# Kernel optimization log

Hardware: AMD Instinct MI355X
Metric: run time of the kernel (lower is better)

## Reference

```python
import jax, jax.numpy as jnp
import numpy as np

DIM = 512; H = 8; TEMP_LEN = 16; TARGET_LEN = 22
NT = TEMP_LEN ** 2          # 256 temp tokens
NS = TARGET_LEN ** 2        # 484 target tokens
N = NT + NS                 # 740
HD = DIM // H
SCALE = HD ** -0.5
EPS = 1e-5
B = 16


def _bias_index(L):
    coords = np.stack(np.meshgrid(np.arange(L), np.arange(L), indexing='ij')).reshape(2, -1)
    rel = (coords[:, :, None] - coords[:, None, :]).transpose(1, 2, 0)  # [L^2, L^2, 2]
    rel[..., 0] += L - 1
    rel[..., 1] += L - 1
    rel[..., 0] *= 2 * L - 1
    return jnp.asarray(rel.sum(-1))  # [L^2, L^2] indices into (2L-1)^2 table

TEMP_IDX = _bias_index(TEMP_LEN)
TARGET_IDX = _bias_index(TARGET_LEN)


def setup_inputs() -> dict:
    key = jax.random.key(0)
    ctr = iter(range(100))
    def nrm(shape, s=1.0):
        return jax.random.normal(jax.random.fold_in(key, next(ctr)), shape, jnp.float32) * s
    def uni(shape):
        return jax.random.uniform(jax.random.fold_in(key, next(ctr)), shape, jnp.float32, 0.5, 1.5)
    d = {'x': nrm((B, N, DIM))}
    for nm in ('q', 'k', 'v'):
        d[f'conv_{nm}_w'] = nrm((DIM, 1, 3, 3), 0.2)   # depthwise 3x3, groups=DIM
        d[f'bn_{nm}_g'] = 1.0 + nrm((DIM,), 0.1)
        d[f'bn_{nm}_b'] = nrm((DIM,), 0.1)
        d[f'bn_{nm}_m'] = nrm((DIM,), 0.1)
        d[f'bn_{nm}_v'] = uni((DIM,))
    for nm in ('q', 'k', 'v', 'p'):
        d[f'w{nm}'] = nrm((DIM, DIM), DIM ** -0.5)
        d[f'b{nm}'] = nrm((DIM,), 0.01)
    d['rpb_target'] = nrm(((2 * TARGET_LEN - 1) ** 2, H), 0.0002)
    d['rpb_temp'] = nrm(((2 * TEMP_LEN - 1) ** 2, 1), 0.0002)
    d['tt_bias'] = nrm((H, 1, NT), 0.0002)       # temp_target_bias_table
    d['tg_tm_bias'] = nrm((H, NS, 1), 0.0002)    # target_temp_bias_table
    return d


def _dwconv_bn(z, w, g, b, m, v):
    # z: [B, C, Hh, Ww]; depthwise conv + BatchNorm2d (inference stats)
    y = jax.lax.conv_general_dilated(z, w, (1, 1), ((1, 1), (1, 1)),
                                     dimension_numbers=('NCHW', 'OIHW', 'NCHW'),
                                     feature_group_count=DIM)
    inv = (g * jax.lax.rsqrt(v + EPS))[None, :, None, None]
    return (y - m[None, :, None, None]) * inv + b[None, :, None, None]


def reference(x, conv_q_w, bn_q_g, bn_q_b, bn_q_m, bn_q_v,
              conv_k_w, bn_k_g, bn_k_b, bn_k_m, bn_k_v,
              conv_v_w, bn_v_g, bn_v_b, bn_v_m, bn_v_v,
              wq, bq, wk, bk, wv, bv, wp, bp,
              rpb_target, rpb_temp, tt_bias, tg_tm_bias):
    Bb = x.shape[0]
    to_img = lambda t, L: t.transpose(0, 2, 1).reshape(Bb, DIM, L, L)
    to_seq = lambda t: t.reshape(Bb, DIM, -1).transpose(0, 2, 1)
    ti = to_img(x[:, :NT], TEMP_LEN)
    tg = to_img(x[:, NT:], TARGET_LEN)

    def conv_branch(w, g, b, m, v):
        return jnp.concatenate([to_seq(_dwconv_bn(ti, w, g, b, m, v)),
                                to_seq(_dwconv_bn(tg, w, g, b, m, v))], axis=1)

    q = conv_branch(conv_q_w, bn_q_g, bn_q_b, bn_q_m, bn_q_v) @ wq + bq
    k = conv_branch(conv_k_w, bn_k_g, bn_k_b, bn_k_m, bn_k_v) @ wk + bk
    v = conv_branch(conv_v_w, bn_v_g, bn_v_b, bn_v_m, bn_v_v) @ wv + bv

    heads = lambda t: t.reshape(Bb, -1, H, HD).transpose(0, 2, 1, 3)
    qtm, ktm, vtm = heads(q[:, :NT]), heads(k[:, :NT]), heads(v[:, :NT])
    qta, kh, vh = heads(q[:, NT:]), heads(k), heads(v)

    # gathered relative-position bias tables
    target_bias = rpb_target[TARGET_IDX.reshape(-1)].reshape(NS, NS, H).transpose(2, 0, 1)  # [H,NS,NS]
    temp_bias = rpb_temp[TEMP_IDX.reshape(-1)].reshape(NT, NT, 1).transpose(2, 0, 1)        # [1,NT,NT]
    padding = tt_bias + tg_tm_bias                                                          # [H,NS,NT]
    rel = jnp.concatenate([padding, target_bias], axis=2)                                   # [H,NS,N]

    # target -> all attention
    attn = jax.nn.softmax(jnp.einsum('bhqd,bhkd->bhqk', qta, kh) * SCALE + rel, axis=-1)
    out_t = jnp.einsum('bhqk,bhkd->bhqd', attn, vh).transpose(0, 2, 1, 3).reshape(Bb, NS, DIM)

    # temp -> temp attention (bias broadcast over heads)
    attn2 = jax.nn.softmax(jnp.einsum('bhqd,bhkd->bhqk', qtm, ktm) * SCALE + temp_bias, axis=-1)
    out_m = jnp.einsum('bhqk,bhkd->bhqd', attn2, vtm).transpose(0, 2, 1, 3).reshape(Bb, NT, DIM)

    return jnp.concatenate([out_m, out_t], axis=1) @ wp + bp
```

## Files before the change

kernel.cpp:

```cpp
#include <hip/hip_runtime.h>
#include <hip/hip_bf16.h>

typedef unsigned short u16;
typedef unsigned int u32;
typedef __attribute__((ext_vector_type(8))) short short8;
typedef __attribute__((ext_vector_type(4))) float f32x4;

#define NTOK 740
#define NTMP 256
#define NTGT 484
#define DM   512
#define MH   8
#define MROWS 11840
#define KPAD 768
#define LOG2E 1.4426950408889634f

__device__ __forceinline__ float b2f(u16 u) {
    union { unsigned int i; float f; } x; x.i = ((unsigned int)u) << 16; return x.f;
}
__device__ __forceinline__ u16 f2b(float f) {
    union { float f; unsigned int i; } x; x.f = f;
    unsigned int r = x.i + 0x7FFFu + ((x.i >> 16) & 1u);
    return (u16)(r >> 16);
}
__device__ __forceinline__ u32 pk2(float a, float b) {
    union { __hip_bfloat162 h; u32 u; } p;
    p.h = __float22bfloat162_rn(float2{a, b});
    return p.u;
}
__device__ __forceinline__ float fexp2(float x) {
    return __builtin_amdgcn_exp2f(x);
}
struct alignas(8) us4 { u16 x, y, z, w; };

__device__ __forceinline__ void gload16(const void* g, void* l) {
    __builtin_amdgcn_global_load_lds(
        (const __attribute__((address_space(1))) void*)g,
        (__attribute__((address_space(3))) void*)l, 16, 0, 0);
}

__global__ __launch_bounds__(256) void transpose4(const float* __restrict__ w0,
                                                  const float* __restrict__ w1,
                                                  const float* __restrict__ w2,
                                                  const float* __restrict__ w3,
                                                  u16* __restrict__ wTbase) {
    __shared__ float t[32][33];
    const int z = blockIdx.z;
    const float* W = z == 0 ? w0 : z == 1 ? w1 : z == 2 ? w2 : w3;
    u16* WT = wTbase + (size_t)z * 262144;
    int bx = blockIdx.x, by = blockIdx.y;
    int tx = threadIdx.x;
    for (int i = threadIdx.y; i < 32; i += 8)
        t[i][tx] = W[(size_t)(by * 32 + i) * 512 + bx * 32 + tx];
    __syncthreads();
    for (int i = threadIdx.y; i < 32; i += 8)
        WT[(size_t)(bx * 32 + i) * 512 + by * 32 + tx] = f2b(t[tx][i]);
}

__global__ __launch_bounds__(512) void prep_conv3(
    const float* __restrict__ cw0, const float* __restrict__ g0, const float* __restrict__ bb0,
    const float* __restrict__ m0, const float* __restrict__ v0,
    const float* __restrict__ cw1, const float* __restrict__ g1, const float* __restrict__ bb1,
    const float* __restrict__ m1, const float* __restrict__ v1,
    const float* __restrict__ cw2, const float* __restrict__ g2, const float* __restrict__ bb2,
    const float* __restrict__ m2, const float* __restrict__ v2,
    float* __restrict__ cwfb, float* __restrict__ shb) {
    const int tap = blockIdx.x, br = blockIdx.y, c = threadIdx.x;
    const float* cw = br == 0 ? cw0 : br == 1 ? cw1 : cw2;
    const float* g  = br == 0 ? g0  : br == 1 ? g1  : g2;
    const float* bb = br == 0 ? bb0 : br == 1 ? bb1 : bb2;
    const float* m  = br == 0 ? m0  : br == 1 ? m1  : m2;
    const float* v  = br == 0 ? v0  : br == 1 ? v1  : v2;
    const float inv = g[c] * rsqrtf(v[c] + 1e-5f);
    cwfb[(br * 9 + tap) * DM + c] = cw[c * 9 + tap] * inv;
    if (tap == 0) shb[br * DM + c] = bb[c] - m[c] * inv;
}

__global__ __launch_bounds__(256) void conv_bn3(
    const float* __restrict__ x,
    const float* __restrict__ cwfb, const float* __restrict__ shb,
    u16* __restrict__ o0, u16* __restrict__ o1, u16* __restrict__ o2) {
    const int bn = blockIdx.x * 2 + (threadIdx.x >> 7);
    const int c = (threadIdx.x & 127) * 4;
    const int b = bn / NTOK, n = bn % NTOK;
    const bool tmp = n < NTMP;
    const int L = tmp ? 16 : 22, base = tmp ? 0 : NTMP, p = n - base;
    const int ph = p / L, pw = p % L;
    float4 xv[9];
#pragma unroll
    for (int tap = 0; tap < 9; ++tap) {
        const int dh = tap / 3 - 1, dw = tap % 3 - 1;
        const int h2 = ph + dh, w2 = pw + dw;
        const bool ok = (h2 >= 0 && h2 < L && w2 >= 0 && w2 < L);
        xv[tap] = ok ? *(const float4*)(x + (size_t)(b * NTOK + base + h2 * L + w2) * DM + c)
                     : float4{0.f, 0.f, 0.f, 0.f};
    }
    const size_t o = (size_t)bn * DM + c;
    u16* out[3] = {o0, o1, o2};
#pragma unroll
    for (int br = 0; br < 3; ++br) {
        float4 acc = *(const float4*)(shb + br * DM + c);
#pragma unroll
        for (int tap = 0; tap < 9; ++tap) {
            const float4 wv = *(const float4*)(cwfb + (br * 9 + tap) * DM + c);
            acc.x = fmaf(wv.x, xv[tap].x, acc.x);
            acc.y = fmaf(wv.y, xv[tap].y, acc.y);
            acc.z = fmaf(wv.z, xv[tap].z, acc.z);
            acc.w = fmaf(wv.w, xv[tap].w, acc.w);
        }
        us4 r;
        r.x = f2b(acc.x); r.y = f2b(acc.y); r.z = f2b(acc.z); r.w = f2b(acc.w);
        *(us4*)(out[br] + o) = r;
    }
}

#define GEMM_BODY(A, BT)                                                             \
    const int tid = threadIdx.x;                                                     \
    const int gm0 = blockIdx.x * 64;                                                 \
    const int gn0 = blockIdx.y * 128;                                                \
    const int lane = tid & 63, w = tid >> 6;                                         \
    const int lr = lane & 15, lg = lane >> 4;                                        \
    const int wm = (w >> 1) * 32, wn = (w & 1) * 64;                                 \
    const int srow4 = lane >> 2;                                                     \
    const int sc = (lane & 3) ^ (srow4 & 3);                                         \
    const u16* asrc  = A  + (size_t)(gm0 + w * 16 + srow4) * 512 + sc * 8;           \
    const u16* bsrc0 = BT + (size_t)(gn0 + w * 32 + srow4) * 512 + sc * 8;           \
    const u16* bsrc1 = BT + (size_t)(gn0 + w * 32 + 16 + srow4) * 512 + sc * 8;      \
    f32x4 acc[2][4] = {};                                                            \
    gload16(asrc, &As[0][w * 512]);                                                  \
    gload16(bsrc0, &Bs[0][w * 1024]);                                                \
    gload16(bsrc1, &Bs[0][w * 1024 + 512]);                                          \
    for (int kt = 0; kt < 16; ++kt) {                                                \
        const int cur = kt & 1;                                                      \
        if (kt < 15) {                                                               \
            gload16(asrc + (kt + 1) * 32, &As[cur ^ 1][w * 512]);                    \
            gload16(bsrc0 + (kt + 1) * 32, &Bs[cur ^ 1][w * 1024]);                  \
            gload16(bsrc1 + (kt + 1) * 32, &Bs[cur ^ 1][w * 1024 + 512]);            \
            asm volatile("s_waitcnt vmcnt(3)" ::: "memory");                         \
        } else {                                                                     \
            asm volatile("s_waitcnt vmcnt(0)" ::: "memory");                         \
        }                                                                            \
        __syncthreads();                                                             \
        short8 af[2], bfr[4];                                                        \
        _Pragma("unroll")                                                            \
        for (int i = 0; i < 2; ++i)                                                  \
            af[i] = *(const short8*)&As[cur][(wm + i * 16 + lr) * 32 + (lg ^ (lr & 3)) * 8]; \
        _Pragma("unroll")                                                            \
        for (int j = 0; j < 4; ++j)                                                  \
            bfr[j] = *(const short8*)&Bs[cur][(wn + j * 16 + lr) * 32 + (lg ^ (lr & 3)) * 8]; \
        _Pragma("unroll")                                                            \
        for (int i = 0; i < 2; ++i)                                                  \
            _Pragma("unroll")                                                        \
            for (int j = 0; j < 4; ++j)                                              \
                acc[i][j] = __builtin_amdgcn_mfma_f32_16x16x32_bf16(af[i], bfr[j], acc[i][j], 0, 0, 0); \
        __syncthreads();                                                             \
    }

__global__ __launch_bounds__(256) void gemm_qkv(
    const u16* __restrict__ Aq, const u16* __restrict__ Ak, const u16* __restrict__ Av,
    const u16* __restrict__ wTb, const float* __restrict__ bq,
    const float* __restrict__ bk, const float* __restrict__ bv,
    u16* __restrict__ qout, u16* __restrict__ kout, u16* __restrict__ vbT, int zbase) {
    __shared__ u16 As[2][64 * 32];
    __shared__ u16 Bs[2][128 * 32];
    const int z = blockIdx.z + zbase;
    const u16* A = z == 0 ? Aq : z == 1 ? Ak : Av;
    const u16* BT = wTb + (size_t)z * 262144;
    const float* bias = z == 0 ? bq : z == 1 ? bk : bv;
    GEMM_BODY(A, BT)
    u16* lin = z == 0 ? qout : kout;
#pragma unroll
    for (int i = 0; i < 2; ++i)
#pragma unroll
        for (int j = 0; j < 4; ++j) {
            const int gc = gn0 + wn + j * 16 + lr;
            const float bvl = bias[gc];
#pragma unroll
            for (int r = 0; r < 4; ++r) {
                const int gr = gm0 + wm + i * 16 + lg * 4 + r;
                const float val = acc[i][j][r] + bvl;
                if (z == 2) {
                    const int b2 = gr / NTOK, k = gr - b2 * NTOK;
                    const int hh = gc >> 6, d = gc & 63;
                    vbT[((size_t)(b2 * MH + hh) * 64 + d) * KPAD + k] = f2b(val);
                } else {
                    lin[(size_t)gr * 512 + gc] = f2b(val);
                }
            }
        }
}

__global__ __launch_bounds__(256) void gemm_out(const u16* __restrict__ Ain,
                                                const u16* __restrict__ BTin,
                                                const float* __restrict__ bias,
                                                float* __restrict__ C) {
    __shared__ u16 As[2][64 * 32];
    __shared__ u16 Bs[2][128 * 32];
    GEMM_BODY(Ain, BTin)
#pragma unroll
    for (int i = 0; i < 2; ++i)
#pragma unroll
        for (int j = 0; j < 4; ++j) {
            const int gc = gn0 + wn + j * 16 + lr;
            const float bvl = bias[gc];
#pragma unroll
            for (int r = 0; r < 4; ++r) {
                const int gr = gm0 + wm + i * 16 + lg * 4 + r;
                C[(size_t)gr * 512 + gc] = acc[i][j][r] + bvl;
            }
        }
}

__global__ __launch_bounds__(256) void build_bias_t(const float* __restrict__ rpb_t,
                                                    const float* __restrict__ tt,
                                                    const float* __restrict__ tg,
                                                    u16* __restrict__ btab) {
    const int q = blockIdx.x, h = blockIdx.y;
    const int qh = q / 22, qw = q % 22;
    const float tgv = tg[h * NTGT + q];
    for (int k = threadIdx.x; k < KPAD; k += 256) {
        float val;
        if (k < NTMP) val = (tt[h * NTMP + k] + tgv) * LOG2E;
        else if (k < NTOK) {
            const int kj = k - NTMP, kh = kj / 22, kw = kj % 22;
            val = rpb_t[((qh - kh + 21) * 43 + (qw - kw + 21)) * MH + h] * LOG2E;
        } else val = -1e30f;
        btab[((size_t)(h * NTGT + q)) * KPAD + k] = f2b(val);
    }
}
__global__ __launch_bounds__(256) void build_bias_m(const float* __restrict__ rpb_m,
                                                    u16* __restrict__ mtab) {
    const int q = blockIdx.x, k = threadIdx.x;
    const int qh = q >> 4, qw = q & 15, kh = k >> 4, kw = k & 15;
    mtab[q * 256 + k] = f2b(rpb_m[(qh - kh + 15) * 31 + (qw - kw + 15)] * LOG2E);
}

__global__ __launch_bounds__(256) void attn_all(const u16* __restrict__ qb,
                                                const u16* __restrict__ kb,
                                                const u16* __restrict__ vbT,
                                                const u16* __restrict__ btab,
                                                const u16* __restrict__ mtab,
                                                u16* __restrict__ attb) {
    __shared__ u16 Ks[2][32][64];
    __shared__ u16 VTs[2][64][32];
    __shared__ u16 Pb[2][4][16][32];

    int wg = blockIdx.x + 6 * (blockIdx.y + 8 * blockIdx.z);
    wg = (wg & 7) * 96 + (wg >> 3);
    const int bx = wg % 6;
    const int hb = wg / 6;
    const int h = hb & 7, b = hb >> 3;

    const bool tgt = bx < 4;
    const int q0 = (tgt ? bx : bx - 4) * 128;
    const int NKr = tgt ? NTOK : NTMP;
    const int NCH = tgt ? 24 : 8;
    const int QTOT = tgt ? NTGT : NTMP;
    const int QOFF = tgt ? NTMP : 0;
    const int TK = tgt ? KPAD : 256;
    const int tid = threadIdx.x;
    const int w = tid >> 6, lane = tid & 63;
    const int lq = lane & 15, lg = lane >> 4;
    const int fq = (lq & 3) ^ ((lq >> 2) & 3);
    const size_t brow = (size_t)b * NTOK;
    const float SCL = 0.125f * LOG2E;

    int qA = q0 + w * 16 + lq;       if (qA > QTOT - 1) qA = QTOT - 1;
    int qB = q0 + 64 + w * 16 + lq;  if (qB > QTOT - 1) qB = QTOT - 1;
    const u16* tbase = tgt ? (btab + (size_t)h * NTGT * KPAD) : mtab;
    const u16* trowA = tbase + (size_t)qA * TK;
    const u16* trowB = tbase + (size_t)qB * TK;

    short8 qfA[2], qfB[2];
#pragma unroll
    for (int dc = 0; dc < 2; ++dc) {
        qfA[dc] = *(const short8*)(qb + (brow + QOFF + qA) * DM + h * 64 + dc * 32 + lg * 8);
        qfB[dc] = *(const short8*)(qb + (brow + QOFF + qB) * DM + h * 64 + dc * 32 + lg * 8);
    }

    const int krow = tid >> 3, ksc = tid & 7;
    const int vrow = tid >> 2, vsc = tid & 3;
    const int fv = (vrow & 3) ^ ((vrow >> 2) & 3);
    const size_t vbase = (size_t)(b * MH + h) * 64 * KPAD;
    const u16* kptr2 = kb + brow * DM + h * 64 + (ksc ^ (krow & 7)) * 8;
    const u16* vptr2 = vbT + vbase + (size_t)vrow * KPAD + (vsc ^ fv) * 8;
    const int NKm1 = NKr - 1;

    float mrunA = -1e30f, lrunA = 0.f, mrunB = -1e30f, lrunB = 0.f;
    f32x4 oTA[4] = {}, oTB[4] = {};

    {
        const int keyc = krow < NKm1 ? krow : NKm1;
        gload16(kptr2 + (size_t)keyc * DM, &Ks[0][w * 8][0]);
        gload16(vptr2, &VTs[0][w * 16][0]);
    }
    us4 bcA0 = *(const us4*)(trowA + lg * 4);
    us4 bcA1 = *(const us4*)(trowA + 16 + lg * 4);
    us4 bcB0 = *(const us4*)(trowB + lg * 4);
    us4 bcB1 = *(const us4*)(trowB + 16 + lg * 4);
    asm volatile("s_waitcnt vmcnt(0)" ::: "memory");
    __syncthreads();

    for (int kc = 0; kc < NCH; ++kc) {
        const int cur = kc & 1, nxt = cur ^ 1;
        const bool more = (kc + 1 < NCH);
        us4 bnA0 = {0,0,0,0}, bnA1 = {0,0,0,0}, bnB0 = {0,0,0,0}, bnB1 = {0,0,0,0};
        if (more) {
            const int key = (kc + 1) * 32 + krow;
            const int keyc = key < NKm1 ? key : NKm1;
            gload16(kptr2 + (size_t)keyc * DM, &Ks[nxt][w * 8][0]);
            gload16(vptr2 + (kc + 1) * 32, &VTs[nxt][w * 16][0]);
            bnA0 = *(const us4*)(trowA + (kc + 1) * 32 + lg * 4);
            bnA1 = *(const us4*)(trowA + (kc + 1) * 32 + 16 + lg * 4);
            bnB0 = *(const us4*)(trowB + (kc + 1) * 32 + lg * 4);
            bnB1 = *(const us4*)(trowB + (kc + 1) * 32 + 16 + lg * 4);
        }

        f32x4 sA0 = {}, sA1 = {}, sB0 = {}, sB1 = {};
        __builtin_amdgcn_s_setprio(1);
#pragma unroll
        for (int dc = 0; dc < 2; ++dc) {
            short8 a0 = *(const short8*)&Ks[cur][lq][((dc * 4 + lg) ^ (lq & 7)) * 8];
            short8 a1 = *(const short8*)&Ks[cur][16 + lq][((dc * 4 + lg) ^ (lq & 7)) * 8];
            sA0 = __builtin_amdgcn_mfma_f32_16x16x32_bf16(a0, qfA[dc], sA0, 0, 0, 0);
            sB0 = __builtin_amdgcn_mfma_f32_16x16x32_bf16(a0, qfB[dc], sB0, 0, 0, 0);
            sA1 = __builtin_amdgcn_mfma_f32_16x16x32_bf16(a1, qfA[dc], sA1, 0, 0, 0);
            sB1 = __builtin_amdgcn_mfma_f32_16x16x32_bf16(a1, qfB[dc], sB1, 0, 0, 0);
        }
        __builtin_amdgcn_s_setprio(0);

        {
            float sv[8];
            sv[0] = fmaf(sA0[0], SCL, b2f(bcA0.x)); sv[1] = fmaf(sA0[1], SCL, b2f(bcA0.y));
            sv[2] = fmaf(sA0[2], SCL, b2f(bcA0.z)); sv[3] = fmaf(sA0[3], SCL, b2f(bcA0.w));
            sv[4] = fmaf(sA1[0], SCL, b2f(bcA1.x)); sv[5] = fmaf(sA1[1], SCL, b2f(bcA1.y));
            sv[6] = fmaf(sA1[2], SCL, b2f(bcA1.z)); sv[7] = fmaf(sA1[3], SCL, b2f(bcA1.w));
            float cm = sv[0];
#pragma unroll
            for (int i = 1; i < 8; ++i) cm = fmaxf(cm, sv[i]);
            cm = fmaxf(cm, __shfl_xor(cm, 16));
            cm = fmaxf(cm, __shfl_xor(cm, 32));
            if (!__all(cm <= mrunA)) {
                const float mnew = fmaxf(mrunA, cm);
                const float alpha = fexp2(mrunA - mnew);
#pragma unroll
                for (int t = 0; t < 4; ++t)
#pragma unroll
                    for (int r = 0; r < 4; ++r) oTA[t][r] *= alpha;
                lrunA *= alpha;
                mrunA = mnew;
            }
            float pv[8], psum = 0.f;
#pragma unroll
            for (int i = 0; i < 8; ++i) { pv[i] = fexp2(sv[i] - mrunA); psum += pv[i]; }
            const int c0 = (((lg >> 1) ^ fq) & 3) * 8 + (lg & 1) * 4;
            const int c1 = (((2 + (lg >> 1)) ^ fq) & 3) * 8 + (lg & 1) * 4;
            *(uint2*)&Pb[0][w][lq][c0] = uint2{pk2(pv[0], pv[1]), pk2(pv[2], pv[3])};
            *(uint2*)&Pb[0][w][lq][c1] = uint2{pk2(pv[4], pv[5]), pk2(pv[6], pv[7])};
            psum += __shfl_xor(psum, 16);
            psum += __shfl_xor(psum, 32);
            lrunA += psum;
        }
        {
            float sv[8];
            sv[0] = fmaf(sB0[0], SCL, b2f(bcB0.x)); sv[1] = fmaf(sB0[1], SCL, b2f(bcB0.y));
            sv[2] = fmaf(sB0[2], SCL, b2f(bcB0.z)); sv[3] = fmaf(sB0[3], SCL, b2f(bcB0.w));
            sv[4] = fmaf(sB1[0], SCL, b2f(bcB1.x)); sv[5] = fmaf(sB1[1], SCL, b2f(bcB1.y));
            sv[6] = fmaf(sB1[2], SCL, b2f(bcB1.z)); sv[7] = fmaf(sB1[3], SCL, b2f(bcB1.w));
            float cm = sv[0];
#pragma unroll
            for (int i = 1; i < 8; ++i) cm = fmaxf(cm, sv[i]);
            cm = fmaxf(cm, __shfl_xor(cm, 16));
            cm = fmaxf(cm, __shfl_xor(cm, 32));
            if (!__all(cm <= mrunB)) {
                const float mnew = fmaxf(mrunB, cm);
                const float alpha = fexp2(mrunB - mnew);
#pragma unroll
                for (int t = 0; t < 4; ++t)
#pragma unroll
                    for (int r = 0; r < 4; ++r) oTB[t][r] *= alpha;
                lrunB *= alpha;
                mrunB = mnew;
            }
            float pv[8], psum = 0.f;
#pragma unroll
            for (int i = 0; i < 8; ++i) { pv[i] = fexp2(sv[i] - mrunB); psum += pv[i]; }
            const int c0 = (((lg >> 1) ^ fq) & 3) * 8 + (lg & 1) * 4;
            const int c1 = (((2 + (lg >> 1)) ^ fq) & 3) * 8 + (lg & 1) * 4;
            *(uint2*)&Pb[1][w][lq][c0] = uint2{pk2(pv[0], pv[1]), pk2(pv[2], pv[3])};
            *(uint2*)&Pb[1][w][lq][c1] = uint2{pk2(pv[4], pv[5]), pk2(pv[6], pv[7])};
            psum += __shfl_xor(psum, 16);
            psum += __shfl_xor(psum, 32);
            lrunB += psum;
        }

        asm volatile("s_waitcnt lgkmcnt(0)" ::: "memory");

        short8 pfA = *(const short8*)&Pb[0][w][lq][((lg ^ fq) & 3) * 8];
        short8 pfB = *(const short8*)&Pb[1][w][lq][((lg ^ fq) & 3) * 8];
        __builtin_amdgcn_s_setprio(1);
#pragma unroll
        for (int t = 0; t < 4; ++t) {
            short8 vf = *(const short8*)&VTs[cur][t * 16 + lq][((lg ^ fq) & 3) * 8];
            oTA[t] = __builtin_amdgcn_mfma_f32_16x16x32_bf16(vf, pfA, oTA[t], 0, 0, 0);
            oTB[t] = __builtin_amdgcn_mfma_f32_16x16x32_bf16(vf, pfB, oTB[t], 0, 0, 0);
        }
        __builtin_amdgcn_s_setprio(0);

        bcA0 = bnA0; bcA1 = bnA1; bcB0 = bnB0; bcB1 = bnB1;
        asm volatile("s_waitcnt vmcnt(0)" ::: "memory");
        __syncthreads();
    }

    {
        const float linv = 1.f / lrunA;
        const int qrow = q0 + w * 16 + lq;
        if (qrow < QTOT) {
            u16* op = attb + (brow + QOFF + qrow) * DM + h * 64;
#pragma unroll
            for (int t = 0; t < 4; ++t)
                *(uint2*)(op + t * 16 + lg * 4) =
                    uint2{pk2(oTA[t][0] * linv, oTA[t][1] * linv),
                          pk2(oTA[t][2] * linv, oTA[t][3] * linv)};
        }
    }
    {
        const float linv = 1.f / lrunB;
        const int qrow = q0 + 64 + w * 16 + lq;
        if (qrow < QTOT) {
            u16* op = attb + (brow + QOFF + qrow) * DM + h * 64;
#pragma unroll
            for (int t = 0; t < 4; ++t)
                *(uint2*)(op + t * 16 + lg * 4) =
                    uint2{pk2(oTB[t][0] * linv, oTB[t][1] * linv),
                          pk2(oTB[t][2] * linv, oTB[t][3] * linv)};
        }
    }
}

extern "C" void kernel_launch(void* const* d_in, const int* in_sizes, int n_in,
                              void* d_out, int out_size, void* d_ws, size_t ws_size,
                              hipStream_t stream) {
    const float* x = (const float*)d_in[0];
    const float* convw[3] = {(const float*)d_in[1], (const float*)d_in[6], (const float*)d_in[11]};
    const float* bng[3]   = {(const float*)d_in[2], (const float*)d_in[7], (const float*)d_in[12]};
    const float* bnb[3]   = {(const float*)d_in[3], (const float*)d_in[8], (const float*)d_in[13]};
    const float* bnm[3]   = {(const float*)d_in[4], (const float*)d_in[9], (const float*)d_in[14]};
    const float* bnv[3]   = {(const float*)d_in[5], (const float*)d_in[10], (const float*)d_in[15]};
    const float* w[4]     = {(const float*)d_in[16], (const float*)d_in[18], (const float*)d_in[20], (const float*)d_in[22]};
    const float* bias[4]  = {(const float*)d_in[17], (const float*)d_in[19], (const float*)d_in[21], (const float*)d_in[23]};
    const float* rpb_t = (const float*)d_in[24];
    const float* rpb_m = (const float*)d_in[25];
    const float* tt    = (const float*)d_in[26];
    const float* tg    = (const float*)d_in[27];

    char* ws = (char*)d_ws;
    u16* wTb = (u16*)ws;
    const size_t SEQ = (size_t)MROWS * DM * 2;
    u16* cbq  = (u16*)(ws + 2097152);
    u16* cbk  = (u16*)(ws + 2097152 + SEQ);
    u16* cbv  = (u16*)(ws + 2097152 + 2 * SEQ);
    u16* kbuf = (u16*)(ws + 2097152 + 3 * SEQ);
    u16* vbT  = (u16*)(ws + 2097152 + 4 * SEQ);
    u16* btab = (u16*)(ws + 2097152 + 4 * SEQ + 12582912);
    u16* mtab = (u16*)(ws + 2097152 + 4 * SEQ + 12582912 + 5947392);
    float* cwf = (float*)(ws + 2097152 + 4 * SEQ + 12582912 + 5947392 + 131072);
    float* shf = cwf + 3 * 9 * DM;
    const size_t off_q2 = 2097152 + 4 * SEQ + 12582912 + 5947392 + 131072 + 61440;
    const bool merged = ws_size >= off_q2 + SEQ;
    u16* qbuf = merged ? (u16*)(ws + off_q2) : cbv;
    u16* attb = cbq;

    transpose4<<<dim3(16, 16, 4), dim3(32, 8), 0, stream>>>(w[0], w[1], w[2], w[3], wTb);
    prep_conv3<<<dim3(9, 3), 512, 0, stream>>>(
        convw[0], bng[0], bnb[0], bnm[0], bnv[0],
        convw[1], bng[1], bnb[1], bnm[1], bnv[1],
        convw[2], bng[2], bnb[2], bnm[2], bnv[2], cwf, shf);
    build_bias_t<<<dim3(NTGT, MH), 256, 0, stream>>>(rpb_t, tt, tg, btab);
    build_bias_m<<<256, 256, 0, stream>>>(rpb_m, mtab);

    conv_bn3<<<MROWS / 2, 256, 0, stream>>>(x, cwf, shf, cbq, cbk, cbv);

    if (merged) {
        gemm_qkv<<<dim3(185, 4, 3), 256, 0, stream>>>(cbq, cbk, cbv, wTb,
                                                      bias[0], bias[1], bias[2],
                                                      qbuf, kbuf, vbT, 0);
    } else {
        gemm_qkv<<<dim3(185, 4, 1), 256, 0, stream>>>(cbq, cbk, cbv, wTb,
                                                      bias[0], bias[1], bias[2],
                                                      qbuf, kbuf, vbT, 2);
        gemm_qkv<<<dim3(185, 4, 2), 256, 0, stream>>>(cbq, cbk, cbv, wTb,
                                                      bias[0], bias[1], bias[2],
                                                      qbuf, kbuf, vbT, 0);
    }

    attn_all<<<dim3(6, 8, 16), 256, 0, stream>>>(qbuf, kbuf, vbT, btab, mtab, attb);

    gemm_out<<<dim3(185, 4), 256, 0, stream>>>(attb, wTb + 3 * 262144, bias[3], (float*)d_out);
}
```

Baseline: 179.1 us.

## Fuse prep kernels into one launch and remap GEMM blocks across XCDs

Merges the four small preprocessing kernels (weight transpose, conv/BN folding, bias table builds) into a single prep_all launch that dispatches on block index. This removes three kernel launches and their gaps. It also remaps GEMM block indices so that consecutive logical tiles land on the same XCD, which is meant to improve L2 reuse of shared A/B tiles. The workspace layout moves to an aligned bump allocator, which may shift buffer offsets slightly.

```diff
diff --git a/kernel.cpp b/kernel.cpp
--- a/kernel.cpp
+++ b/kernel.cpp
@@ -39,41 +39,64 @@
         (__attribute__((address_space(3))) void*)l, 16, 0, 0);
 }
 
-__global__ __launch_bounds__(256) void transpose4(const float* __restrict__ w0,
-                                                  const float* __restrict__ w1,
-                                                  const float* __restrict__ w2,
-                                                  const float* __restrict__ w3,
-                                                  u16* __restrict__ wTbase) {
-    __shared__ float t[32][33];
-    const int z = blockIdx.z;
-    const float* W = z == 0 ? w0 : z == 1 ? w1 : z == 2 ? w2 : w3;
-    u16* WT = wTbase + (size_t)z * 262144;
-    int bx = blockIdx.x, by = blockIdx.y;
-    int tx = threadIdx.x;
-    for (int i = threadIdx.y; i < 32; i += 8)
-        t[i][tx] = W[(size_t)(by * 32 + i) * 512 + bx * 32 + tx];
-    __syncthreads();
-    for (int i = threadIdx.y; i < 32; i += 8)
-        WT[(size_t)(bx * 32 + i) * 512 + by * 32 + tx] = f2b(t[tx][i]);
-}
-
-__global__ __launch_bounds__(512) void prep_conv3(
+__global__ __launch_bounds__(256) void prep_all(
+    const float* __restrict__ w0, const float* __restrict__ w1,
+    const float* __restrict__ w2, const float* __restrict__ w3, u16* __restrict__ wTbase,
     const float* __restrict__ cw0, const float* __restrict__ g0, const float* __restrict__ bb0,
     const float* __restrict__ m0, const float* __restrict__ v0,
     const float* __restrict__ cw1, const float* __restrict__ g1, const float* __restrict__ bb1,
     const float* __restrict__ m1, const float* __restrict__ v1,
     const float* __restrict__ cw2, const float* __restrict__ g2, const float* __restrict__ bb2,
     const float* __restrict__ m2, const float* __restrict__ v2,
-    float* __restrict__ cwfb, float* __restrict__ shb) {
-    const int tap = blockIdx.x, br = blockIdx.y, c = threadIdx.x;
-    const float* cw = br == 0 ? cw0 : br == 1 ? cw1 : cw2;
-    const float* g  = br == 0 ? g0  : br == 1 ? g1  : g2;
-    const float* bb = br == 0 ? bb0 : br == 1 ? bb1 : bb2;
-    const float* m  = br == 0 ? m0  : br == 1 ? m1  : m2;
-    const float* v  = br == 0 ? v0  : br == 1 ? v1  : v2;
-    const float inv = g[c] * rsqrtf(v[c] + 1e-5f);
-    cwfb[(br * 9 + tap) * DM + c] = cw[c * 9 + tap] * inv;
-    if (tap == 0) shb[br * DM + c] = bb[c] - m[c] * inv;
+    float* __restrict__ cwfb, float* __restrict__ shb,
+    const float* __restrict__ rpb_t, const float* __restrict__ tt,
+    const float* __restrict__ tg, u16* __restrict__ btab,
+    const float* __restrict__ rpb_m, u16* __restrict__ mtab) {
+    __shared__ float t[32][33];
+    const int id = blockIdx.x, tid = threadIdx.x;
+    if (id < 1024) {
+        const int z = id >> 8, rem = id & 255;
+        const int bx = rem & 15, by = rem >> 4;
+        const float* W = z == 0 ? w0 : z == 1 ? w1 : z == 2 ? w2 : w3;
+        u16* WT = wTbase + (size_t)z * 262144;
+        const int tx = tid & 31, ty = tid >> 5;
+        for (int i = ty; i < 32; i += 8)
+            t[i][tx] = W[(size_t)(by * 32 + i) * 512 + bx * 32 + tx];
+        __syncthreads();
+        for (int i = ty; i < 32; i += 8)
+            WT[(size_t)(bx * 32 + i) * 512 + by * 32 + tx] = f2b(t[tx][i]);
+    } else if (id < 1051) {
+        const int rem = id - 1024;
+        const int tap = rem % 9, br = rem / 9;
+        const float* cw = br == 0 ? cw0 : br == 1 ? cw1 : cw2;
+        const float* g  = br == 0 ? g0  : br == 1 ? g1  : g2;
+        const float* bb = br == 0 ? bb0 : br == 1 ? bb1 : bb2;
+        const float* m  = br == 0 ? m0  : br == 1 ? m1  : m2;
+        const float* v  = br == 0 ? v0  : br == 1 ? v1  : v2;
+        for (int c = tid; c < DM; c += 256) {
+            const float inv = g[c] * rsqrtf(v[c] + 1e-5f);
+            cwfb[(br * 9 + tap) * DM + c] = cw[c * 9 + tap] * inv;
+            if (tap == 0) shb[br * DM + c] = bb[c] - m[c] * inv;
+        }
+    } else if (id < 4923) {
+        const int rem = id - 1051;
+        const int h = rem / NTGT, q = rem % NTGT;
+        const int qh = q / 22, qw = q % 22;
+        const float tgv = tg[h * NTGT + q];
+        for (int k = tid; k < KPAD; k += 256) {
+            float val;
+            if (k < NTMP) val = (tt[h * NTMP + k] + tgv) * LOG2E;
+            else if (k < NTOK) {
+                const int kj = k - NTMP, kh = kj / 22, kw = kj % 22;
+                val = rpb_t[((qh - kh + 21) * 43 + (qw - kw + 21)) * MH + h] * LOG2E;
+            } else val = -1e30f;
+            btab[((size_t)(h * NTGT + q)) * KPAD + k] = f2b(val);
+        }
+    } else {
+        const int q = id - 4923, k = tid;
+        const int qh = q >> 4, qw = q & 15, kh = k >> 4, kw = k & 15;
+        mtab[q * 256 + k] = f2b(rpb_m[(qh - kh + 15) * 31 + (qw - kw + 15)] * LOG2E);
+    }
 }
 
 __global__ __launch_bounds__(256) void conv_bn3(
@@ -116,8 +139,6 @@
 
 #define GEMM_BODY(A, BT)                                                             \
     const int tid = threadIdx.x;                                                     \
-    const int gm0 = blockIdx.x * 64;                                                 \
-    const int gn0 = blockIdx.y * 128;                                                \
     const int lane = tid & 63, w = tid >> 6;                                         \
     const int lr = lane & 15, lg = lane >> 4;                                        \
     const int wm = (w >> 1) * 32, wn = (w & 1) * 64;                                 \
@@ -156,14 +177,25 @@
         __syncthreads();                                                             \
     }
 
+__device__ __forceinline__ int xcd_remap(int hw, int n) {
+    const int q8 = n >> 3, r8 = n & 7;
+    const int xcd = hw & 7, i8 = hw >> 3;
+    return (xcd < r8 ? xcd * (q8 + 1) : r8 * (q8 + 1) + (xcd - r8) * q8) + i8;
+}
+
 __global__ __launch_bounds__(256) void gemm_qkv(
     const u16* __restrict__ Aq, const u16* __restrict__ Ak, const u16* __restrict__ Av,
     const u16* __restrict__ wTb, const float* __restrict__ bq,
     const float* __restrict__ bk, const float* __restrict__ bv,
     u16* __restrict__ qout, u16* __restrict__ kout, u16* __restrict__ vbT, int zbase) {
-    __shared__ u16 As[2][64 * 32];
-    __shared__ u16 Bs[2][128 * 32];
-    const int z = blockIdx.z + zbase;
+    __shared__ u16 As[2][2048];
+    __shared__ u16 Bs[2][4096];
+    const int hw = blockIdx.x + 185 * (blockIdx.y + 4 * blockIdx.z);
+    const int lid = xcd_remap(hw, 740 * gridDim.z);
+    const int by = lid & 3;
+    const int bx = (lid >> 2) % 185;
+    const int z = lid / 740 + zbase;
+    const int gm0 = bx * 64, gn0 = by * 128;
     const u16* A = z == 0 ? Aq : z == 1 ? Ak : Av;
     const u16* BT = wTb + (size_t)z * 262144;
     const float* bias = z == 0 ? bq : z == 1 ? bk : bv;
@@ -194,8 +226,13 @@
                                                 const u16* __restrict__ BTin,
                                                 const float* __restrict__ bias,
                                                 float* __restrict__ C) {
-    __shared__ u16 As[2][64 * 32];
-    __shared__ u16 Bs[2][128 * 32];
+    __shared__ u16 As[2][2048];
+    __shared__ u16 Bs[2][4096];
+    const int hw = blockIdx.x + 185 * blockIdx.y;
+    const int lid = xcd_remap(hw, 740);
+    const int by = lid & 3;
+    const int bx = lid >> 2;
+    const int gm0 = bx * 64, gn0 = by * 128;
     GEMM_BODY(Ain, BTin)
 #pragma unroll
     for (int i = 0; i < 2; ++i)
@@ -209,30 +246,6 @@
                 C[(size_t)gr * 512 + gc] = acc[i][j][r] + bvl;
             }
         }
-}
-
-__global__ __launch_bounds__(256) void build_bias_t(const float* __restrict__ rpb_t,
-                                                    const float* __restrict__ tt,
-                                                    const float* __restrict__ tg,
-                                                    u16* __restrict__ btab) {
-    const int q = blockIdx.x, h = blockIdx.y;
-    const int qh = q / 22, qw = q % 22;
-    const float tgv = tg[h * NTGT + q];
-    for (int k = threadIdx.x; k < KPAD; k += 256) {
-        float val;
-        if (k < NTMP) val = (tt[h * NTMP + k] + tgv) * LOG2E;
-        else if (k < NTOK) {
-            const int kj = k - NTMP, kh = kj / 22, kw = kj % 22;
-            val = rpb_t[((qh - kh + 21) * 43 + (qw - kw + 21)) * MH + h] * LOG2E;
-        } else val = -1e30f;
-        btab[((size_t)(h * NTGT + q)) * KPAD + k] = f2b(val);
-    }
-}
-__global__ __launch_bounds__(256) void build_bias_m(const float* __restrict__ rpb_m,
-                                                    u16* __restrict__ mtab) {
-    const int q = blockIdx.x, k = threadIdx.x;
-    const int qh = q >> 4, qw = q & 15, kh = k >> 4, kw = k & 15;
-    mtab[q * 256 + k] = f2b(rpb_m[(qh - kh + 15) * 31 + (qw - kw + 15)] * LOG2E);
 }
 
 __global__ __launch_bounds__(256) void attn_all(const u16* __restrict__ qb,
@@ -454,30 +467,30 @@
     const float* tt    = (const float*)d_in[26];
     const float* tg    = (const float*)d_in[27];
 
-    char* ws = (char*)d_ws;
-    u16* wTb = (u16*)ws;
+    char* p = (char*)d_ws;
+    auto alloc = [&](size_t n) { char* r = p; p += (n + 255) & ~(size_t)255; return r; };
     const size_t SEQ = (size_t)MROWS * DM * 2;
-    u16* cbq  = (u16*)(ws + 2097152);
-    u16* cbk  = (u16*)(ws + 2097152 + SEQ);
-    u16* cbv  = (u16*)(ws + 2097152 + 2 * SEQ);
-    u16* kbuf = (u16*)(ws + 2097152 + 3 * SEQ);
-    u16* vbT  = (u16*)(ws + 2097152 + 4 * SEQ);
-    u16* btab = (u16*)(ws + 2097152 + 4 * SEQ + 12582912);
-    u16* mtab = (u16*)(ws + 2097152 + 4 * SEQ + 12582912 + 5947392);
-    float* cwf = (float*)(ws + 2097152 + 4 * SEQ + 12582912 + 5947392 + 131072);
-    float* shf = cwf + 3 * 9 * DM;
-    const size_t off_q2 = 2097152 + 4 * SEQ + 12582912 + 5947392 + 131072 + 61440;
-    const bool merged = ws_size >= off_q2 + SEQ;
-    u16* qbuf = merged ? (u16*)(ws + off_q2) : cbv;
+    u16* wTb  = (u16*)alloc(4 * 524288);
+    u16* cbq  = (u16*)alloc(SEQ);
+    u16* cbk  = (u16*)alloc(SEQ);
+    u16* cbv  = (u16*)alloc(SEQ);
+    u16* kbuf = (u16*)alloc(SEQ);
+    u16* vbT  = (u16*)alloc((size_t)16 * MH * 64 * KPAD * 2);
+    u16* btab = (u16*)alloc((size_t)MH * NTGT * KPAD * 2);
+    u16* mtab = (u16*)alloc(256 * 256 * 2);
+    float* cwf = (float*)alloc(3 * 9 * DM * 4);
+    float* shf = (float*)alloc(3 * DM * 4);
+    const size_t used = (size_t)(p - (char*)d_ws);
+    const bool merged = ws_size >= used + SEQ;
+    u16* qbuf = merged ? (u16*)alloc(SEQ) : cbv;
     u16* attb = cbq;
 
-    transpose4<<<dim3(16, 16, 4), dim3(32, 8), 0, stream>>>(w[0], w[1], w[2], w[3], wTb);
-    prep_conv3<<<dim3(9, 3), 512, 0, stream>>>(
+    prep_all<<<5179, 256, 0, stream>>>(
+        w[0], w[1], w[2], w[3], wTb,
         convw[0], bng[0], bnb[0], bnm[0], bnv[0],
         convw[1], bng[1], bnb[1], bnm[1], bnv[1],
-        convw[2], bng[2], bnb[2], bnm[2], bnv[2], cwf, shf);
-    build_bias_t<<<dim3(NTGT, MH), 256, 0, stream>>>(rpb_t, tt, tg, btab);
-    build_bias_m<<<256, 256, 0, stream>>>(rpb_m, mtab);
+        convw[2], bng[2], bnb[2], bnm[2], bnv[2], cwf, shf,
+        rpb_t, tt, tg, btab, rpb_m, mtab);
 
     conv_bn3<<<MROWS / 2, 256, 0, stream>>>(x, cwf, shf, cbq, cbk, cbv);
 
```

Result: no change. 178.7 us (-0.3%).
